# Optimization experiments

Hardware: AMD Instinct MI355X
Metric: run time of the kernel (lower is better)

## Reference

```python
import jax, jax.numpy as jnp
import numpy as np

N_NODES = 50000
N_EDGES = 1600000
IN_CH = 64
EDGE_DIM = 32
NUM_HID = 256
NUM_CLASSES = 16
NUM_GRAPHS = 512


def setup_inputs() -> dict:
    key = jax.random.key(0)
    ks = jax.random.split(key, 16)
    z_dim = 2 * IN_CH + EDGE_DIM
    s = lambda k, shp, fan: jax.random.normal(k, shp, dtype=jnp.float32) * (1.0 / np.sqrt(fan))
    return {
        "x": jax.random.normal(ks[0], (N_NODES, IN_CH), dtype=jnp.float32),
        "edge_index": jax.random.randint(ks[1], (2, N_EDGES), 0, N_NODES, dtype=jnp.int64),
        "edge_attr": jax.random.normal(ks[2], (N_EDGES, EDGE_DIM), dtype=jnp.float32),
        "batch": jnp.sort(jax.random.randint(ks[3], (N_NODES,), 0, NUM_GRAPHS, dtype=jnp.int64)),
        # CGConv layer 1 (lin_f: gate, lin_s: filter)
        "w_f1": s(ks[4], (IN_CH, z_dim), z_dim), "b_f1": jnp.zeros((IN_CH,), jnp.float32),
        "w_s1": s(ks[5], (IN_CH, z_dim), z_dim), "b_s1": jnp.zeros((IN_CH,), jnp.float32),
        # CGConv layer 2
        "w_f2": s(ks[6], (IN_CH, z_dim), z_dim), "b_f2": jnp.zeros((IN_CH,), jnp.float32),
        "w_s2": s(ks[7], (IN_CH, z_dim), z_dim), "b_s2": jnp.zeros((IN_CH,), jnp.float32),
        # MLP
        "w1": s(ks[8], (NUM_HID, IN_CH), IN_CH), "b1": jnp.zeros((NUM_HID,), jnp.float32),
        "w2": s(ks[9], (NUM_CLASSES, NUM_HID), NUM_HID), "b2": jnp.zeros((NUM_CLASSES,), jnp.float32),
    }


def _cgconv(x, src, dst, edge_attr, w_f, b_f, w_s, b_s, inv_deg):
    # z = [x_i, x_j, e_ij] per edge (j -> i), shape [E, 2C+D]
    z = jnp.concatenate([x[dst], x[src], edge_attr], axis=1)
    msg = jax.nn.sigmoid(z @ w_f.T + b_f) * jax.nn.softplus(z @ w_s.T + b_s)
    agg = jax.ops.segment_sum(msg, dst, num_segments=N_NODES) * inv_deg[:, None]
    return agg + x  # residual connection in CGConv


def reference(x, edge_index, edge_attr, batch,
              w_f1, b_f1, w_s1, b_s1, w_f2, b_f2, w_s2, b_s2,
              w1, b1, w2, b2):
    src, dst = edge_index[0], edge_index[1]
    deg = jax.ops.segment_sum(jnp.ones((src.shape[0],), x.dtype), dst, num_segments=N_NODES)
    inv_deg = 1.0 / jnp.maximum(deg, 1.0)

    h = _cgconv(x, src, dst, edge_attr, w_f1, b_f1, w_s1, b_s1, inv_deg)
    h = _cgconv(h, src, dst, edge_attr, w_f2, b_f2, w_s2, b_s2, inv_deg)

    # scatter_mean over graphs
    gsum = jax.ops.segment_sum(h, batch, num_segments=NUM_GRAPHS)
    gcnt = jax.ops.segment_sum(jnp.ones((h.shape[0],), h.dtype), batch, num_segments=NUM_GRAPHS)
    g = gsum / jnp.maximum(gcnt, 1.0)[:, None]

    out = jax.nn.relu(g @ w1.T + b1) @ w2.T + b2
    return jax.nn.log_softmax(out, axis=1)
```

## Files before the change

kernel.cpp:

```cpp
#include <hip/hip_runtime.h>
#include <hip/hip_bf16.h>

#define N_NODES 50000
#define N_EDGES 1600000
#define IN_CH 64
#define NUM_HID 256
#define NUM_CLASSES 16
#define NUM_GRAPHS 512
#define NBS 196

typedef short bf16x8 __attribute__((ext_vector_type(8)));
typedef float f32x4 __attribute__((ext_vector_type(4)));

#if __has_builtin(__builtin_amdgcn_rcpf)
#define RCPF(x) __builtin_amdgcn_rcpf(x)
#else
#define RCPF(x) (1.0f / (x))
#endif

__device__ inline unsigned short f2b(float f) {
    unsigned int u = __float_as_uint(f);
    unsigned int r = (u + 0x7FFF + ((u >> 16) & 1)) >> 16;
    return (unsigned short)r;
}
__device__ inline float b2f(unsigned short u) {
    return __uint_as_float(((unsigned int)u) << 16);
}

__device__ inline void gl16(const unsigned short* g, unsigned short* l) {
    __builtin_amdgcn_global_load_lds(
        (const __attribute__((address_space(1))) unsigned int*)g,
        (__attribute__((address_space(3))) unsigned int*)l, 16, 0, 0);
}

__global__ void prep_w_kernel(const float* __restrict__ wf1, const float* __restrict__ ws1,
                              const float* __restrict__ wf2, const float* __restrict__ ws2,
                              unsigned short* __restrict__ wb1, unsigned short* __restrict__ wb2) {
    int i = blockIdx.x * 256 + threadIdx.x;
    if (i >= 128 * 160) return;
    int r = i / 160, k = i - r * 160;
    wb1[i] = f2b(r < 64 ? wf1[r * 160 + k] : ws1[(r - 64) * 160 + k]);
    wb2[i] = f2b(r < 64 ? wf2[r * 160 + k] : ws2[(r - 64) * 160 + k]);
}

__global__ void prep_x_kernel(const float4* __restrict__ x, unsigned short* __restrict__ xb) {
    int i = blockIdx.x * 256 + threadIdx.x;
    if (i >= N_NODES * 16) return;
    float4 v = x[i];
    ushort4 u; u.x = f2b(v.x); u.y = f2b(v.y); u.z = f2b(v.z); u.w = f2b(v.w);
    *(ushort4*)(xb + i * 4) = u;
}

__global__ void hist_kernel(const int* __restrict__ ei, int* __restrict__ cnt) {
    int i = blockIdx.x * 256 + threadIdx.x;
    if (i < N_EDGES) atomicAdd(&cnt[ei[N_EDGES + i]], 1);
}

__global__ void bsum_kernel(const int* __restrict__ cnt, int* __restrict__ bsum) {
    __shared__ int sm[256];
    int i = blockIdx.x * 256 + threadIdx.x;
    sm[threadIdx.x] = (i < N_NODES) ? cnt[i] : 0;
    __syncthreads();
    for (int off = 128; off > 0; off >>= 1) {
        if (threadIdx.x < off) sm[threadIdx.x] += sm[threadIdx.x + off];
        __syncthreads();
    }
    if (threadIdx.x == 0) bsum[blockIdx.x] = sm[0];
}

__global__ void bscan_kernel(const int* __restrict__ bsum, int* __restrict__ boffs) {
    __shared__ int sm[256];
    int t = threadIdx.x;
    int v = (t < NBS) ? bsum[t] : 0;
    sm[t] = v; __syncthreads();
    for (int off = 1; off < 256; off <<= 1) {
        int u = (t >= off) ? sm[t - off] : 0;
        __syncthreads();
        sm[t] += u;
        __syncthreads();
    }
    if (t < NBS) boffs[t] = sm[t] - v;
}

__global__ void apply_kernel(const int* __restrict__ cnt, const int* __restrict__ boffs,
                             int* __restrict__ cursor, float* __restrict__ invdeg) {
    __shared__ int sm[256];
    int t = threadIdx.x, i = blockIdx.x * 256 + t;
    int c = (i < N_NODES) ? cnt[i] : 0;
    sm[t] = c; __syncthreads();
    for (int off = 1; off < 256; off <<= 1) {
        int u = (t >= off) ? sm[t - off] : 0;
        __syncthreads();
        sm[t] += u;
        __syncthreads();
    }
    if (i < N_NODES) {
        cursor[i] = boffs[blockIdx.x] + sm[t] - c;
        invdeg[i] = 1.0f / fmaxf((float)c, 1.0f);
    }
}

__global__ void scatter_kernel(const int* __restrict__ ei, int* __restrict__ cursor,
                               const float* __restrict__ ea,
                               int2* __restrict__ sed, unsigned short* __restrict__ eab) {
    int e = blockIdx.x * 256 + threadIdx.x;
    if (e >= N_EDGES) return;
    int s = ei[e], d = ei[N_EDGES + e];
    int p = atomicAdd(&cursor[d], 1);
    sed[p] = make_int2(s, d);
    const float4* src = (const float4*)(ea + (size_t)e * 32);
    unsigned short* dst = eab + (size_t)p * 32;
    #pragma unroll
    for (int j = 0; j < 8; ++j) {
        float4 v = src[j];
        ushort4 u; u.x = f2b(v.x); u.y = f2b(v.y); u.z = f2b(v.z); u.w = f2b(v.w);
        *(ushort4*)(dst + j * 4) = u;
    }
}

__global__ __launch_bounds__(256, 2)
void edge_mfma(const unsigned short* __restrict__ xb,
               const int2* __restrict__ sed, const unsigned short* __restrict__ eab,
               const unsigned short* __restrict__ wb,
               const float* __restrict__ bfv, const float* __restrict__ bsv,
               float* __restrict__ agg)
{
    __shared__ __align__(16) unsigned short Zd[2][64 * 64];
    __shared__ __align__(16) unsigned short Zs[2][64 * 64];
    __shared__ __align__(16) unsigned short Ze[2][64 * 32];

    const int tid = threadIdx.x;
    const int w = tid >> 6, lane = tid & 63, lr = lane & 15, lq = lane >> 4;
    const int chw = w * 16;

    bf16x8 B[2][5];
    #pragma unroll
    for (int mat = 0; mat < 2; ++mat)
        #pragma unroll
        for (int ks = 0; ks < 5; ++ks)
            B[mat][ks] = *(const bf16x8*)(wb + (size_t)(mat * 64 + chw + lr) * 160 + ks * 32 + lq * 8);

    const float biasF = bfv[chw + lr];
    const float biasS = bsv[chw + lr];

    const int NT = N_EDGES / 64;
    const int nblk = gridDim.x;

    #define STAGE(T, PAR) do { \
        int e0_ = (T) * 64; \
        int rb_ = w * 16 + (lane >> 3); \
        int dcA_ = (lane & 7) ^ (lane >> 3); \
        int2 s0_ = sed[e0_ + rb_]; \
        int2 s1_ = sed[e0_ + rb_ + 8]; \
        gl16(xb + (size_t)s0_.y * 64 + dcA_ * 8, &Zd[PAR][w * 1024]); \
        gl16(xb + (size_t)s1_.y * 64 + dcA_ * 8, &Zd[PAR][w * 1024 + 512]); \
        gl16(xb + (size_t)s0_.x * 64 + dcA_ * 8, &Zs[PAR][w * 1024]); \
        gl16(xb + (size_t)s1_.x * 64 + dcA_ * 8, &Zs[PAR][w * 1024 + 512]); \
        int rE_ = w * 16 + (lane >> 2); \
        int dcE_ = (lane & 3) ^ ((lane >> 3) & 3); \
        gl16(eab + (size_t)(e0_ + rE_) * 32 + dcE_ * 8, &Ze[PAR][w * 512]); \
    } while (0)

    int t = blockIdx.x;
    if (t < NT) STAGE(t, 0);
    __syncthreads();
    int par = 0;

    for (; t < NT; t += nblk) {
        int tn = t + nblk;
        if (tn < NT) STAGE(tn, par ^ 1);

        int dme = sed[t * 64 + lane].y;

        f32x4 aF[4] = {}; f32x4 aS[4] = {};
        #pragma unroll
        for (int ks = 0; ks < 5; ++ks) {
            bf16x8 a[4];
            #pragma unroll
            for (int m = 0; m < 4; ++m) {
                const int rm = m * 16 + lr;
                if (ks < 2) {
                    int j = ks * 4 + lq;
                    a[m] = *(const bf16x8*)&Zd[par][rm * 64 + ((j ^ (rm & 7)) * 8)];
                } else if (ks < 4) {
                    int j = (ks - 2) * 4 + lq;
                    a[m] = *(const bf16x8*)&Zs[par][rm * 64 + ((j ^ (rm & 7)) * 8)];
                } else {
                    a[m] = *(const bf16x8*)&Ze[par][rm * 32 + ((lq ^ ((rm >> 1) & 3)) * 8)];
                }
            }
            #pragma unroll
            for (int m = 0; m < 4; ++m) {
                aF[m] = __builtin_amdgcn_mfma_f32_16x16x32_bf16(a[m], B[0][ks], aF[m], 0, 0, 0);
                aS[m] = __builtin_amdgcn_mfma_f32_16x16x32_bf16(a[m], B[1][ks], aS[m], 0, 0, 0);
            }
        }

        float val[16];
        #pragma unroll
        for (int m = 0; m < 4; ++m)
            #pragma unroll
            for (int i = 0; i < 4; ++i) {
                float f = aF[m][i] + biasF;
                float s = aS[m][i] + biasS;
                float sig = RCPF(1.0f + __expf(-f));
                float sp = fmaxf(s, 0.0f) + __logf(1.0f + __expf(-fabsf(s)));
                val[m * 4 + i] = sig * sp;
            }

        {
            int dprev = __shfl(dme, lane - 1);
            unsigned long long bmask = __ballot((lane == 0) || (dme != dprev));
            while (bmask) {
                int lo = (int)__builtin_ctzll(bmask);
                bmask &= bmask - 1;
                int hi = bmask ? (int)__builtin_ctzll(bmask) : 64;
                int dst = __shfl(dme, lo);
                float t0 = 0.0f;
                #pragma unroll
                for (int m = 0; m < 4; ++m)
                    #pragma unroll
                    for (int i = 0; i < 4; ++i) {
                        int r = m * 16 + lq * 4 + i;
                        t0 += ((r >= lo) && (r < hi)) ? val[m * 4 + i] : 0.0f;
                    }
                t0 += __shfl_xor(t0, 16);
                t0 += __shfl_xor(t0, 32);
                if (lq == 0)
                    atomicAdd(&agg[(size_t)dst * 64 + chw + lr], t0);
            }
        }

        __syncthreads();
        par ^= 1;
    }
    #undef STAGE
}

__global__ void resid2_kernel(const float4* __restrict__ agg, const float* __restrict__ inv_deg,
                              const float4* __restrict__ x, unsigned short* __restrict__ hb)
{
    int i = blockIdx.x * 256 + threadIdx.x;
    if (i >= N_NODES * 16) return;
    int n = i >> 4;
    float iv = inv_deg[n];
    float4 a = agg[i], xv = x[i];
    ushort4 u;
    u.x = f2b(a.x * iv + xv.x); u.y = f2b(a.y * iv + xv.y);
    u.z = f2b(a.z * iv + xv.z); u.w = f2b(a.w * iv + xv.w);
    *(ushort4*)(hb + i * 4) = u;
}

__global__ void pool2_kernel(const float* __restrict__ agg, const float* __restrict__ inv_deg,
                             const unsigned short* __restrict__ hb, const int* __restrict__ batch,
                             float* __restrict__ gsum, float* __restrict__ gcnt)
{
    const int ch = threadIdx.x & 63, sub = threadIdx.x >> 6;
    const int base = blockIdx.x * 64 + sub * 16;
    float acc = 0.0f;
    int gcur = -1, rl = 0;
    #pragma unroll
    for (int j = 0; j < 16; ++j) {
        int n = base + j;
        if (n >= N_NODES) break;
        int g = batch[n];
        float v = agg[(size_t)n * 64 + ch] * inv_deg[n] + b2f(hb[(size_t)n * 64 + ch]);
        if (g != gcur) {
            if (gcur >= 0) {
                atomicAdd(&gsum[gcur * 64 + ch], acc);
                if (ch == 0) atomicAdd(&gcnt[gcur], (float)rl);
            }
            gcur = g; acc = v; rl = 1;
        } else {
            acc += v; rl++;
        }
    }
    if (gcur >= 0) {
        atomicAdd(&gsum[gcur * 64 + ch], acc);
        if (ch == 0) atomicAdd(&gcnt[gcur], (float)rl);
    }
}

__global__ __launch_bounds__(64)
void head_kernel(const float* __restrict__ gsum, const float* __restrict__ gcnt,
                 const float* __restrict__ w1, const float* __restrict__ b1,
                 const float* __restrict__ w2, const float* __restrict__ b2,
                 float* __restrict__ out)
{
    __shared__ float gv[64];
    __shared__ float hid[256];
    __shared__ float outv[16];
    const int g = blockIdx.x, t = threadIdx.x;
    float cnt = fmaxf(gcnt[g], 1.0f);
    gv[t] = gsum[g * 64 + t] / cnt;
    __syncthreads();
    #pragma unroll
    for (int r = 0; r < 4; ++r) {
        int c = t + r * 64;
        float acc = b1[c];
        const float4* wr = (const float4*)(w1 + c * 64);
        const float4* gvv = (const float4*)gv;
        #pragma unroll
        for (int k = 0; k < 16; ++k) {
            float4 wv = wr[k], xv = gvv[k];
            acc += wv.x * xv.x + wv.y * xv.y + wv.z * xv.z + wv.w * xv.w;
        }
        hid[c] = fmaxf(acc, 0.0f);
    }
    __syncthreads();
    if (t < 16) {
        float acc = b2[t];
        const float4* wr = (const float4*)(w2 + t * 256);
        const float4* hv = (const float4*)hid;
        for (int k = 0; k < 64; ++k) {
            float4 wv = wr[k], xv = hv[k];
            acc += wv.x * xv.x + wv.y * xv.y + wv.z * xv.z + wv.w * xv.w;
        }
        outv[t] = acc;
    }
    __syncthreads();
    if (t < 16) {
        float m = outv[0];
        #pragma unroll
        for (int j = 1; j < 16; ++j) m = fmaxf(m, outv[j]);
        float ssum = 0.0f;
        #pragma unroll
        for (int j = 0; j < 16; ++j) ssum += expf(outv[j] - m);
        out[g * 16 + t] = outv[t] - m - logf(ssum);
    }
}

extern "C" void kernel_launch(void* const* d_in, const int* in_sizes, int n_in,
                              void* d_out, int out_size, void* d_ws, size_t ws_size,
                              hipStream_t stream)
{
    const float* x     = (const float*)d_in[0];
    const int*   ei    = (const int*)d_in[1];
    const float* ea    = (const float*)d_in[2];
    const int*   batch = (const int*)d_in[3];
    const float* wf1 = (const float*)d_in[4];
    const float* bf1 = (const float*)d_in[5];
    const float* ws1 = (const float*)d_in[6];
    const float* bs1 = (const float*)d_in[7];
    const float* wf2 = (const float*)d_in[8];
    const float* bf2 = (const float*)d_in[9];
    const float* ws2 = (const float*)d_in[10];
    const float* bs2 = (const float*)d_in[11];
    const float* w1 = (const float*)d_in[12];
    const float* b1 = (const float*)d_in[13];
    const float* w2 = (const float*)d_in[14];
    const float* b2 = (const float*)d_in[15];
    float* out = (float*)d_out;

    char* ws = (char*)d_ws;
    int*   cnt    = (int*)(ws + 0x0000000);
    int*   cursor = (int*)(ws + 0x0040000);
    float* invdeg = (float*)(ws + 0x0080000);
    int*   bsum   = (int*)(ws + 0x00C0000);
    int*   boffs  = (int*)(ws + 0x00C1000);
    int2*  sed    = (int2*)(ws + 0x0100000);
    unsigned short* xb  = (unsigned short*)(ws + 0x1500000);
    unsigned short* hb  = (unsigned short*)(ws + 0x1C00000);
    float* agg = (float*)(ws + 0x2300000);
    unsigned short* wb1 = (unsigned short*)(ws + 0x3000000);
    unsigned short* wb2 = (unsigned short*)(ws + 0x3010000);
    float* gsum = (float*)(ws + 0x3020000);
    float* gcnt = (float*)(ws + 0x3040000);
    unsigned short* eab = (unsigned short*)(ws + 0x3100000);

    hipMemsetAsync(cnt, 0, 200000, stream);
    hipMemsetAsync(agg, 0, 12800000, stream);
    hipMemsetAsync(gsum, 0, 131072 + 2048, stream);

    prep_w_kernel<<<80, 256, 0, stream>>>(wf1, ws1, wf2, ws2, wb1, wb2);
    prep_x_kernel<<<3125, 256, 0, stream>>>((const float4*)x, xb);
    hist_kernel<<<6250, 256, 0, stream>>>(ei, cnt);
    bsum_kernel<<<NBS, 256, 0, stream>>>(cnt, bsum);
    bscan_kernel<<<1, 256, 0, stream>>>(bsum, boffs);
    apply_kernel<<<NBS, 256, 0, stream>>>(cnt, boffs, cursor, invdeg);
    scatter_kernel<<<6250, 256, 0, stream>>>(ei, cursor, ea, sed, eab);

    edge_mfma<<<1024, 256, 0, stream>>>(xb, sed, eab, wb1, bf1, bs1, agg);
    resid2_kernel<<<3125, 256, 0, stream>>>((const float4*)agg, invdeg, (const float4*)x, hb);
    hipMemsetAsync(agg, 0, 12800000, stream);
    edge_mfma<<<1024, 256, 0, stream>>>(hb, sed, eab, wb2, bf2, bs2, agg);
    pool2_kernel<<<782, 256, 0, stream>>>(agg, invdeg, hb, batch, gsum, gcnt);
    head_kernel<<<NUM_GRAPHS, 64, 0, stream>>>(gsum, gcnt, w1, b1, w2, b2, out);
}
```

Measured before the change: 610.4 us.

## Restage edge messages through LDS and segment-reduce per wave over edges

Edge messages are written to a padded shared-memory tile, and each wave then walks its 16 edges sequentially per channel, accumulating runs of equal destination and issuing one atomic per run. This replaces the ballot/shuffle run detection with its masked 16-term sum and cross-lane shuffles, and destination indices are now prefetched into LDS during staging. It adds an extra block barrier with an LDS round trip, and each wave only merges runs within its 16-edge slice, so atomics can rise if edges are sorted by destination.

```diff
diff --git a/kernel.cpp b/kernel.cpp
--- a/kernel.cpp
+++ b/kernel.cpp
@@ -128,6 +128,8 @@
     __shared__ __align__(16) unsigned short Zd[2][64 * 64];
     __shared__ __align__(16) unsigned short Zs[2][64 * 64];
     __shared__ __align__(16) unsigned short Ze[2][64 * 32];
+    __shared__ float msg[64 * 68];
+    __shared__ int dstl[2][64];
 
     const int tid = threadIdx.x;
     const int w = tid >> 6, lane = tid & 63, lr = lane & 15, lq = lane >> 4;
@@ -159,6 +161,12 @@
         int rE_ = w * 16 + (lane >> 2); \
         int dcE_ = (lane & 3) ^ ((lane >> 3) & 3); \
         gl16(eab + (size_t)(e0_ + rE_) * 32 + dcE_ * 8, &Ze[PAR][w * 512]); \
+        if (tid < 64) dstl[PAR][tid] = sed[e0_ + tid].y; \
+    } while (0)
+
+    #define SOFT_BARRIER() do { \
+        asm volatile("s_waitcnt lgkmcnt(0)" ::: "memory"); \
+        __builtin_amdgcn_s_barrier(); \
     } while (0)
 
     int t = blockIdx.x;
@@ -169,8 +177,6 @@
     for (; t < NT; t += nblk) {
         int tn = t + nblk;
         if (tn < NT) STAGE(tn, par ^ 1);
-
-        int dme = sed[t * 64 + lane].y;
 
         f32x4 aF[4] = {}; f32x4 aS[4] = {};
         #pragma unroll
@@ -196,7 +202,6 @@
             }
         }
 
-        float val[16];
         #pragma unroll
         for (int m = 0; m < 4; ++m)
             #pragma unroll
@@ -205,36 +210,33 @@
                 float s = aS[m][i] + biasS;
                 float sig = RCPF(1.0f + __expf(-f));
                 float sp = fmaxf(s, 0.0f) + __logf(1.0f + __expf(-fabsf(s)));
-                val[m * 4 + i] = sig * sp;
-            }
+                msg[(m * 16 + lq * 4 + i) * 68 + chw + lr] = sig * sp;
+            }
+        SOFT_BARRIER();
 
         {
-            int dprev = __shfl(dme, lane - 1);
-            unsigned long long bmask = __ballot((lane == 0) || (dme != dprev));
-            while (bmask) {
-                int lo = (int)__builtin_ctzll(bmask);
-                bmask &= bmask - 1;
-                int hi = bmask ? (int)__builtin_ctzll(bmask) : 64;
-                int dst = __shfl(dme, lo);
-                float t0 = 0.0f;
-                #pragma unroll
-                for (int m = 0; m < 4; ++m)
-                    #pragma unroll
-                    for (int i = 0; i < 4; ++i) {
-                        int r = m * 16 + lq * 4 + i;
-                        t0 += ((r >= lo) && (r < hi)) ? val[m * 4 + i] : 0.0f;
-                    }
-                t0 += __shfl_xor(t0, 16);
-                t0 += __shfl_xor(t0, 32);
-                if (lq == 0)
-                    atomicAdd(&agg[(size_t)dst * 64 + chw + lr], t0);
-            }
+            float acc = 0.0f;
+            int dcur = dstl[par][w * 16];
+            #pragma unroll
+            for (int j = 0; j < 16; ++j) {
+                int e = w * 16 + j;
+                int d = dstl[par][e];
+                float v = msg[e * 68 + lane];
+                if (d != dcur) {
+                    atomicAdd(&agg[(size_t)dcur * 64 + lane], acc);
+                    dcur = d; acc = v;
+                } else {
+                    acc += v;
+                }
+            }
+            atomicAdd(&agg[(size_t)dcur * 64 + lane], acc);
         }
 
         __syncthreads();
         par ^= 1;
     }
     #undef STAGE
+    #undef SOFT_BARRIER
 }
 
 __global__ void resid2_kernel(const float4* __restrict__ agg, const float* __restrict__ inv_deg,
```

Result: faster. 596.6 us (-2.3%).

## Restructure edge MFMA kernel to per-wave 16-edge tiles with LDS-resident weights

Applied to the files above, without the earlier changes.

Replaces the block-wide 64-edge tile, whose gathered rows were double-buffered through LDS with async global-to-LDS loads, by independent per-wave 16-edge tiles. Each lane now gathers its node and edge rows straight into registers, and the full weight matrix is staged once in LDS and read per MFMA. This removes per-iteration __syncthreads and the LDS staging of activations. In exchange it loses the prefetch/compute overlap, adds LDS reads of weights for every tile, and shrinks segments so more atomic adds are issued.

```diff
diff --git a/kernel.cpp b/kernel.cpp
--- a/kernel.cpp
+++ b/kernel.cpp
@@ -25,12 +25,6 @@
 }
 __device__ inline float b2f(unsigned short u) {
     return __uint_as_float(((unsigned int)u) << 16);
-}
-
-__device__ inline void gl16(const unsigned short* g, unsigned short* l) {
-    __builtin_amdgcn_global_load_lds(
-        (const __attribute__((address_space(1))) unsigned int*)g,
-        (__attribute__((address_space(3))) unsigned int*)l, 16, 0, 0);
 }
 
 __global__ void prep_w_kernel(const float* __restrict__ wf1, const float* __restrict__ ws1,
@@ -125,116 +119,94 @@
                const float* __restrict__ bfv, const float* __restrict__ bsv,
                float* __restrict__ agg)
 {
-    __shared__ __align__(16) unsigned short Zd[2][64 * 64];
-    __shared__ __align__(16) unsigned short Zs[2][64 * 64];
-    __shared__ __align__(16) unsigned short Ze[2][64 * 32];
+    __shared__ __align__(16) unsigned short Bl[40 * 64 * 8];
 
     const int tid = threadIdx.x;
-    const int w = tid >> 6, lane = tid & 63, lr = lane & 15, lq = lane >> 4;
-    const int chw = w * 16;
-
-    bf16x8 B[2][5];
+    const int lane = tid & 63, lr = lane & 15, lq = lane >> 4;
+
+    for (int j = tid; j < 40 * 64; j += 256) {
+        int f = j >> 6, ls = j & 63;
+        int lq2 = ls >> 4, lr2 = ls & 15;
+        int mat = f / 20, rem = f - mat * 20, chb = rem / 5, ks = rem - chb * 5;
+        bf16x8 v = *(const bf16x8*)(wb + (size_t)(mat * 64 + chb * 16 + lr2) * 160 + ks * 32 + lq2 * 8);
+        *(bf16x8*)&Bl[(size_t)j * 8] = v;
+    }
+    __syncthreads();
+
+    float biasF[4], biasS[4];
     #pragma unroll
-    for (int mat = 0; mat < 2; ++mat)
-        #pragma unroll
-        for (int ks = 0; ks < 5; ++ks)
-            B[mat][ks] = *(const bf16x8*)(wb + (size_t)(mat * 64 + chw + lr) * 160 + ks * 32 + lq * 8);
-
-    const float biasF = bfv[chw + lr];
-    const float biasS = bsv[chw + lr];
-
-    const int NT = N_EDGES / 64;
-    const int nblk = gridDim.x;
-
-    #define STAGE(T, PAR) do { \
-        int e0_ = (T) * 64; \
-        int rb_ = w * 16 + (lane >> 3); \
-        int dcA_ = (lane & 7) ^ (lane >> 3); \
-        int2 s0_ = sed[e0_ + rb_]; \
-        int2 s1_ = sed[e0_ + rb_ + 8]; \
-        gl16(xb + (size_t)s0_.y * 64 + dcA_ * 8, &Zd[PAR][w * 1024]); \
-        gl16(xb + (size_t)s1_.y * 64 + dcA_ * 8, &Zd[PAR][w * 1024 + 512]); \
-        gl16(xb + (size_t)s0_.x * 64 + dcA_ * 8, &Zs[PAR][w * 1024]); \
-        gl16(xb + (size_t)s1_.x * 64 + dcA_ * 8, &Zs[PAR][w * 1024 + 512]); \
-        int rE_ = w * 16 + (lane >> 2); \
-        int dcE_ = (lane & 3) ^ ((lane >> 3) & 3); \
-        gl16(eab + (size_t)(e0_ + rE_) * 32 + dcE_ * 8, &Ze[PAR][w * 512]); \
-    } while (0)
-
-    int t = blockIdx.x;
-    if (t < NT) STAGE(t, 0);
-    __syncthreads();
-    int par = 0;
-
-    for (; t < NT; t += nblk) {
-        int tn = t + nblk;
-        if (tn < NT) STAGE(tn, par ^ 1);
-
-        int dme = sed[t * 64 + lane].y;
+    for (int chb = 0; chb < 4; ++chb) {
+        biasF[chb] = bfv[chb * 16 + lr];
+        biasS[chb] = bsv[chb * 16 + lr];
+    }
+
+    const int NT16 = N_EDGES / 16;
+    const int wg = blockIdx.x * 4 + (tid >> 6);
+    const int wstride = gridDim.x * 4;
+    const int lq4 = lq * 4;
+
+    for (int T = wg; T < NT16; T += wstride) {
+        const int e0 = T * 16;
+        int2 sd = sed[e0 + lr];
+        const int dme = sd.y, sme = sd.x;
+
+        bf16x8 ad0 = *(const bf16x8*)(xb + (size_t)dme * 64 + lq * 8);
+        bf16x8 ad1 = *(const bf16x8*)(xb + (size_t)dme * 64 + 32 + lq * 8);
+        bf16x8 as0 = *(const bf16x8*)(xb + (size_t)sme * 64 + lq * 8);
+        bf16x8 as1 = *(const bf16x8*)(xb + (size_t)sme * 64 + 32 + lq * 8);
+        bf16x8 ae  = *(const bf16x8*)(eab + (size_t)(e0 + lr) * 32 + lq * 8);
 
         f32x4 aF[4] = {}; f32x4 aS[4] = {};
         #pragma unroll
         for (int ks = 0; ks < 5; ++ks) {
-            bf16x8 a[4];
+            bf16x8 a = (ks == 0) ? ad0 : (ks == 1) ? ad1 : (ks == 2) ? as0 : (ks == 3) ? as1 : ae;
             #pragma unroll
-            for (int m = 0; m < 4; ++m) {
-                const int rm = m * 16 + lr;
-                if (ks < 2) {
-                    int j = ks * 4 + lq;
-                    a[m] = *(const bf16x8*)&Zd[par][rm * 64 + ((j ^ (rm & 7)) * 8)];
-                } else if (ks < 4) {
-                    int j = (ks - 2) * 4 + lq;
-                    a[m] = *(const bf16x8*)&Zs[par][rm * 64 + ((j ^ (rm & 7)) * 8)];
-                } else {
-                    a[m] = *(const bf16x8*)&Ze[par][rm * 32 + ((lq ^ ((rm >> 1) & 3)) * 8)];
-                }
+            for (int chb = 0; chb < 4; ++chb) {
+                bf16x8 b0 = *(const bf16x8*)&Bl[(size_t)((0 * 20 + chb * 5 + ks) * 64 + lane) * 8];
+                bf16x8 b1 = *(const bf16x8*)&Bl[(size_t)((1 * 20 + chb * 5 + ks) * 64 + lane) * 8];
+                aF[chb] = __builtin_amdgcn_mfma_f32_16x16x32_bf16(a, b0, aF[chb], 0, 0, 0);
+                aS[chb] = __builtin_amdgcn_mfma_f32_16x16x32_bf16(a, b1, aS[chb], 0, 0, 0);
             }
-            #pragma unroll
-            for (int m = 0; m < 4; ++m) {
-                aF[m] = __builtin_amdgcn_mfma_f32_16x16x32_bf16(a[m], B[0][ks], aF[m], 0, 0, 0);
-                aS[m] = __builtin_amdgcn_mfma_f32_16x16x32_bf16(a[m], B[1][ks], aS[m], 0, 0, 0);
-            }
         }
 
         float val[16];
         #pragma unroll
-        for (int m = 0; m < 4; ++m)
+        for (int chb = 0; chb < 4; ++chb)
             #pragma unroll
             for (int i = 0; i < 4; ++i) {
-                float f = aF[m][i] + biasF;
-                float s = aS[m][i] + biasS;
+                float f = aF[chb][i] + biasF[chb];
+                float s = aS[chb][i] + biasS[chb];
                 float sig = RCPF(1.0f + __expf(-f));
                 float sp = fmaxf(s, 0.0f) + __logf(1.0f + __expf(-fabsf(s)));
-                val[m * 4 + i] = sig * sp;
+                val[chb * 4 + i] = sig * sp;
             }
 
         {
             int dprev = __shfl(dme, lane - 1);
-            unsigned long long bmask = __ballot((lane == 0) || (dme != dprev));
+            unsigned long long bmask = __ballot((lr == 0) || (dme != dprev)) & 0xFFFFull;
             while (bmask) {
                 int lo = (int)__builtin_ctzll(bmask);
                 bmask &= bmask - 1;
-                int hi = bmask ? (int)__builtin_ctzll(bmask) : 64;
+                int hi = bmask ? (int)__builtin_ctzll(bmask) : 16;
                 int dst = __shfl(dme, lo);
-                float t0 = 0.0f;
+                float tc[4];
                 #pragma unroll
-                for (int m = 0; m < 4; ++m)
+                for (int chb = 0; chb < 4; ++chb) {
+                    float s = 0.0f;
                     #pragma unroll
                     for (int i = 0; i < 4; ++i) {
-                        int r = m * 16 + lq * 4 + i;
-                        t0 += ((r >= lo) && (r < hi)) ? val[m * 4 + i] : 0.0f;
+                        int r = lq4 + i;
+                        s += ((r >= lo) && (r < hi)) ? val[chb * 4 + i] : 0.0f;
                     }
-                t0 += __shfl_xor(t0, 16);
-                t0 += __shfl_xor(t0, 32);
-                if (lq == 0)
-                    atomicAdd(&agg[(size_t)dst * 64 + chw + lr], t0);
+                    s += __shfl_xor(s, 16);
+                    s += __shfl_xor(s, 32);
+                    tc[chb] = s;
+                }
+                float tsel = (lq == 0) ? tc[0] : (lq == 1) ? tc[1] : (lq == 2) ? tc[2] : tc[3];
+                atomicAdd(&agg[(size_t)dst * 64 + lq * 16 + lr], tsel);
             }
         }
-
-        __syncthreads();
-        par ^= 1;
-    }
-    #undef STAGE
+    }
 }
 
 __global__ void resid2_kernel(const float4* __restrict__ agg, const float* __restrict__ inv_deg,
```

After: 547.7 us. 1.11x faster.
